# Kernel optimization log

Hardware: AMD Instinct MI355X
Metric: run time of the kernel (lower is better)

Reference implementation:

```python
import jax, jax.numpy as jnp
import numpy as np

B, N, D, H, EF = 8, 1024, 768, 8, 4
S = D * EF          # sparse_dim = 3072
HD = S // H         # head_dim = 384
HUB_POW = 1.5
PERSIST = 0.95
EPS = 1e-6
LN_EPS = 1e-5


def setup_inputs() -> dict:
    key = jax.random.key(0)
    ks = jax.random.split(key, 8)
    s = 0.02  # weight init scale
    return {
        "x": jax.random.normal(ks[0], (B, N, D), jnp.float32),
        "memory": jax.random.normal(ks[1], (H, HD, HD), jnp.float32) * 0.01,
        "ln_g": jnp.ones((D,), jnp.float32),
        "ln_b": jnp.zeros((D,), jnp.float32),
        "w_in": jax.random.normal(ks[2], (D, 3 * S), jnp.float32) * s,
        "b_in": jnp.zeros((3 * S,), jnp.float32),
        "w_out": jax.random.normal(ks[3], (S, D), jnp.float32) * s,
        "b_out": jnp.zeros((D,), jnp.float32),
        "w_rg": jax.random.normal(ks[4], (D, H), jnp.float32) * s,
        "b_rg": jnp.zeros((H,), jnp.float32),
        "w_wg": jax.random.normal(ks[5], (D, H), jnp.float32) * s,
        "b_wg": jnp.zeros((H,), jnp.float32),
        "w_res": jax.random.normal(ks[6], (D, 1), jnp.float32) * s,
        "b_res": jnp.zeros((1,), jnp.float32),
    }


def reference(x, memory, ln_g, ln_b, w_in, b_in, w_out, b_out,
              w_rg, b_rg, w_wg, b_wg, w_res, b_res):
    residual = x
    # LayerNorm (biased variance, matching torch)
    mu = x.mean(axis=-1, keepdims=True)
    var = x.var(axis=-1, keepdims=True)
    xn = (x - mu) / jnp.sqrt(var + LN_EPS) * ln_g + ln_b

    qkv = xn @ w_in + b_in                      # [B,N,3S]
    q, k, v = jnp.split(qkv, 3, axis=-1)

    def to_heads(t):                            # [B,N,S] -> [B,H,N,hd]
        return t.reshape(B, N, H, HD).transpose(0, 2, 1, 3)

    # power-law hub feature map
    q = jnp.power(jax.nn.relu(to_heads(q)) + EPS, HUB_POW)
    k = jnp.power(jax.nn.relu(to_heads(k)) + EPS, HUB_POW)
    v = to_heads(v)
    # normalize k over the token axis
    k = k / (k.sum(axis=2, keepdims=True) + EPS)

    # per-head linear-attention state: k^T @ v -> [B,H,hd,hd]
    batch_state = jnp.einsum('bhnd,bhne->bhde', k, v)

    x_mean = xn.mean(axis=1)                    # [B,D]
    read = jax.nn.sigmoid(x_mean @ w_rg + b_rg)[:, :, None, None]   # [B,H,1,1]
    write = jax.nn.sigmoid(x_mean @ w_wg + b_wg)[:, :, None, None]  # [B,H,1,1]
    residue = jax.nn.sigmoid(xn @ w_res + b_res)                    # [B,N,1]

    # gated EMA memory update (update happens BEFORE read, as in source)
    state_mean = batch_state.mean(axis=0)       # [H,hd,hd]
    mem_new = PERSIST * memory + (1.0 - PERSIST) * write.mean(axis=0) * state_mean

    # read from updated persistent memory
    y = jnp.einsum('bhnd,bhde->bhne', q, mem_new[None] * read)
    y = y.transpose(0, 2, 1, 3).reshape(B, N, S)

    out = residue * (y @ w_out + b_out) + (1.0 - residue) * residual
    return out
```

## Files before the change

### kernel.cpp

```cpp
#include <hip/hip_runtime.h>
#include <hip/hip_bf16.h>
#include <cstdint>
#include <cstddef>


typedef __bf16 bf16_t;
typedef bf16_t bf16x4 __attribute__((ext_vector_type(4)));
typedef bf16_t bf16x8 __attribute__((ext_vector_type(8)));
typedef float f32x4 __attribute__((ext_vector_type(4)));

__device__ __forceinline__ void gemm128_bt(
    const bf16_t* __restrict__ A, int lda,
    const bf16_t* __restrict__ BT, int ldb,
    int K, int row0, int col0,
    bf16_t* As, bf16_t* Bs, f32x4 acc[4][4])
{
    const int t    = threadIdx.x;
    const int lane = t & 63;
    const int wid  = t >> 6;
    const int wr   = wid >> 1, wc = wid & 1;
    const int fr   = lane & 15;
    const int fk   = (lane >> 4) * 8;

#pragma unroll
    for (int m = 0; m < 4; ++m)
#pragma unroll
        for (int n = 0; n < 4; ++n)
            acc[m][n] = (f32x4){0.f, 0.f, 0.f, 0.f};

    const int rr = lane >> 2;
    const int rc = (lane & 3) * 8;

    for (int k0 = 0; k0 < K; k0 += 32) {
#pragma unroll
        for (int c = 0; c < 2; ++c) {
            const int q = wid * 2 + c;
            __builtin_amdgcn_global_load_lds(
                (const __attribute__((address_space(1))) void*)(A + (size_t)(row0 + q * 16 + rr) * lda + (k0 + rc)),
                (__attribute__((address_space(3))) void*)(As + q * 512), 16, 0, 0);
            __builtin_amdgcn_global_load_lds(
                (const __attribute__((address_space(1))) void*)(BT + (size_t)(col0 + q * 16 + rr) * ldb + (k0 + rc)),
                (__attribute__((address_space(3))) void*)(Bs + q * 512), 16, 0, 0);
        }
        __syncthreads();

        bf16x8 av[4], bv[4];
#pragma unroll
        for (int m = 0; m < 4; ++m)
            av[m] = *(const bf16x8*)&As[(wr * 64 + m * 16 + fr) * 32 + fk];
#pragma unroll
        for (int n = 0; n < 4; ++n)
            bv[n] = *(const bf16x8*)&Bs[(wc * 64 + n * 16 + fr) * 32 + fk];
#pragma unroll
        for (int m = 0; m < 4; ++m)
#pragma unroll
            for (int n = 0; n < 4; ++n)
                acc[m][n] = __builtin_amdgcn_mfma_f32_16x16x32_bf16(av[m], bv[n], acc[m][n], 0, 0, 0);
        __syncthreads();
    }
}

__device__ __forceinline__ void band_map(int flat, int nby, int& bx, int& by)
{
    const int xcd = flat & 7;
    const int seq = flat >> 3;
    const int bandsz = nby >> 3;
    by = xcd * bandsz + (seq % bandsz);
    bx = seq / bandsz;
}


__global__ void ktrans_w(const float* __restrict__ in, bf16_t* __restrict__ out, int R, int C)
{
    __shared__ float tl[32][33];
    const int c0 = blockIdx.x * 32, r0 = blockIdx.y * 32;
    const int tx = threadIdx.x, ty = threadIdx.y;
#pragma unroll
    for (int i = ty; i < 32; i += 8) tl[i][tx] = in[(size_t)(r0 + i) * C + c0 + tx];
    __syncthreads();
#pragma unroll
    for (int i = ty; i < 32; i += 8) out[(size_t)(c0 + i) * R + r0 + tx] = (bf16_t)tl[tx][i];
}

__device__ __forceinline__ float block_sum256(float v, float* s4)
{
#pragma unroll
    for (int off = 32; off > 0; off >>= 1) v += __shfl_down(v, off);
    const int lane = threadIdx.x & 63, w = threadIdx.x >> 6;
    if (lane == 0) s4[w] = v;
    __syncthreads();
    return s4[0] + s4[1] + s4[2] + s4[3];
}

__global__ void __launch_bounds__(256) kln(
    const float* __restrict__ x, const float* __restrict__ g, const float* __restrict__ bt,
    const float* __restrict__ w_res, const float* __restrict__ b_res,
    bf16_t* __restrict__ xn, float* __restrict__ residue)
{
    __shared__ float red[12];
    const int row = blockIdx.x;
    const float* xr = x + (size_t)row * 768;
    const int t = threadIdx.x;
    const float v0 = xr[t], v1 = xr[t + 256], v2 = xr[t + 512];
    const float ts  = block_sum256(v0 + v1 + v2, red);
    const float ts2 = block_sum256(v0 * v0 + v1 * v1 + v2 * v2, red + 4);
    const float mu  = ts * (1.f / 768.f);
    const float var = ts2 * (1.f / 768.f) - mu * mu;
    const float rs  = rsqrtf(var + 1e-5f);
    float dot = 0.f;
    {
        float xv;
        xv = (v0 - mu) * rs * g[t]       + bt[t];       xn[(size_t)row * 768 + t]       = (bf16_t)xv; dot += xv * w_res[t];
        xv = (v1 - mu) * rs * g[t + 256] + bt[t + 256]; xn[(size_t)row * 768 + t + 256] = (bf16_t)xv; dot += xv * w_res[t + 256];
        xv = (v2 - mu) * rs * g[t + 512] + bt[t + 512]; xn[(size_t)row * 768 + t + 512] = (bf16_t)xv; dot += xv * w_res[t + 512];
    }
    const float td = block_sum256(dot, red + 8);
    if (t == 0) residue[row] = 1.f / (1.f + expf(-(td + b_res[0])));
}

__global__ void kcolmean(const bf16_t* __restrict__ xn, float* __restrict__ xmean)
{
    const int b = blockIdx.x, dc = blockIdx.y, nc = blockIdx.z;
    const int d = dc * 256 + threadIdx.x;
    const bf16_t* p = xn + (size_t)(b * 1024 + nc * 128) * 768 + d;
    float s = 0.f;
#pragma unroll 4
    for (int n = 0; n < 128; ++n) s += (float)p[(size_t)n * 768];
    atomicAdd(&xmean[b * 768 + d], s);
}

__global__ void __launch_bounds__(256) kgates(
    const float* __restrict__ xmean,
    const float* __restrict__ w_rg, const float* __restrict__ b_rg,
    const float* __restrict__ w_wg, const float* __restrict__ b_wg,
    float* __restrict__ read_g, float* __restrict__ wmean)
{
    __shared__ float pr[64][4], pw[64][4], wg[64];
    const int t = threadIdx.x, grp = t >> 2, qtr = t & 3;
    const int b = grp >> 3, h = grp & 7;
    float dr = 0.f, dw = 0.f;
    for (int d = qtr * 192; d < qtr * 192 + 192; ++d) {
        const float xm = xmean[b * 768 + d] * (1.f / 1024.f);
        dr += xm * w_rg[d * 8 + h];
        dw += xm * w_wg[d * 8 + h];
    }
    pr[grp][qtr] = dr; pw[grp][qtr] = dw;
    __syncthreads();
    if (qtr == 0) {
        const float sr = pr[grp][0] + pr[grp][1] + pr[grp][2] + pr[grp][3];
        const float sw = pw[grp][0] + pw[grp][1] + pw[grp][2] + pw[grp][3];
        read_g[grp] = 1.f / (1.f + expf(-(sr + b_rg[h])));
        wg[grp]     = 1.f / (1.f + expf(-(sw + b_wg[h])));
    }
    __syncthreads();
    if (t < 8) {
        float s = 0.f;
#pragma unroll
        for (int b2 = 0; b2 < 8; ++b2) s += wg[b2 * 8 + t];
        wmean[t] = s * 0.125f;
    }
}

__global__ void __launch_bounds__(512, 2) kgemm_qkv256(
    const bf16_t* __restrict__ xnc, const bf16_t* __restrict__ w_inT,
    const float* __restrict__ b_in,
    bf16_t* __restrict__ qfc, bf16_t* __restrict__ kTc, bf16_t* __restrict__ vTc,
    float* __restrict__ ksum_c, int nrt )
{
    __shared__ __align__(16) bf16_t L[65536];
    const int t = threadIdx.x, lane = t & 63, wid = t >> 6;
    const int wr = wid >> 2, wc = wid & 3;
    int bx, by;
    band_map(blockIdx.y * 36 + blockIdx.x, nrt, bx, by);
    const int row0 = by * 256, col0 = bx * 256;

    f32x4 acc[8][4];
#pragma unroll
    for (int m = 0; m < 8; ++m)
#pragma unroll
        for (int n = 0; n < 4; ++n)
            acc[m][n] = (f32x4){0.f, 0.f, 0.f, 0.f};

    const int grow = 16 * wid + (lane >> 2);
    const int gcol = (lane & 3) * 8;
    const int ldst = 512 * wid + 8 * lane;

    auto stage = [&](int buf, int k0) {
        bf16_t* base = &L[buf * 32768];
#pragma unroll
        for (int op = 0; op < 2; ++op) {
            const bf16_t* src = op ? w_inT : xnc;
            const int r0 = op ? col0 : row0;
#pragma unroll
            for (int s = 0; s < 2; ++s)
#pragma unroll
                for (int j = 0; j < 2; ++j)
                    __builtin_amdgcn_global_load_lds(
                        (const __attribute__((address_space(1))) void*)(src + (size_t)(r0 + 128 * j + grow) * 768 + (k0 + 32 * s + gcol)),
                        (__attribute__((address_space(3))) void*)(base + op * 16384 + s * 8192 + j * 4096 + ldst),
                        16, 0, 0);
        }
    };

    const int fr = lane & 15, fo = (lane >> 4) * 8;

    stage(0, 0);
    __syncthreads();
    int cur = 0;
    for (int k0 = 0; k0 < 768; k0 += 64) {
        if (k0 + 64 < 768) stage(cur ^ 1, k0 + 64);
        const bf16_t* base = &L[cur * 32768];
#pragma unroll
        for (int s = 0; s < 2; ++s) {
            bf16x8 bv[4];
#pragma unroll
            for (int n = 0; n < 4; ++n)
                bv[n] = *(const bf16x8*)&base[16384 + s * 8192 + (wc * 64 + n * 16 + fr) * 32 + fo];
#pragma unroll
            for (int m = 0; m < 8; ++m) {
                const bf16x8 av = *(const bf16x8*)&base[s * 8192 + (wr * 128 + m * 16 + fr) * 32 + fo];
#pragma unroll
                for (int n = 0; n < 4; ++n)
                    acc[m][n] = __builtin_amdgcn_mfma_f32_16x16x32_bf16(av, bv[n], acc[m][n], 0, 0, 0);
            }
        }
        __syncthreads();
        cur ^= 1;
    }

    const int third = col0 / 3072;
    if (third == 0) {
#pragma unroll
        for (int m = 0; m < 8; ++m) {
#pragma unroll
            for (int n2 = 0; n2 < 4; ++n2) {
                const int col  = col0 + wc * 64 + n2 * 16 + fr;
                const float bias = b_in[col];
#pragma unroll
                for (int r = 0; r < 4; ++r) {
                    const int row = row0 + wr * 128 + m * 16 + (lane >> 4) * 4 + r;
                    const float v = acc[m][n2][r] + bias;
                    const float u = fmaxf(v, 0.f) + 1e-6f;
                    qfc[(size_t)row * 3072 + col] = (bf16_t)(u * sqrtf(u));
                }
            }
        }
    } else {
        const int lb  = row0 >> 10;
        const int nbb = (row0 & 1023) + wr * 128 + (lane >> 4) * 4;
#pragma unroll
        for (int n2 = 0; n2 < 4; ++n2) {
            const int colg = col0 + wc * 64 + n2 * 16 + fr;
            const int coll = colg - third * 3072;
            const int h = coll / 384, d = coll % 384;
            bf16_t* dstT = ((third == 1) ? kTc : vTc) + (size_t)(lb * 8 + h) * 393216;
            const float bias = b_in[colg];
            float ksp = 0.f;
#pragma unroll
            for (int m = 0; m < 8; ++m) {
                bf16x4 pk;
#pragma unroll
                for (int r = 0; r < 4; ++r) {
                    float v = acc[m][n2][r] + bias;
                    if (third == 1) { const float u = fmaxf(v, 0.f) + 1e-6f; v = u * sqrtf(u); ksp += v; }
                    pk[r] = (bf16_t)v;
                }
                *(bf16x4*)&dstT[(size_t)d * 1024 + nbb + m * 16] = pk;
            }
            if (third == 1) atomicAdd(&ksum_c[(size_t)(lb * 8 + h) * 384 + d], ksp);
        }
    }
}

__global__ void __launch_bounds__(256) kgemm_state(
    const bf16_t* __restrict__ kTc, const bf16_t* __restrict__ vTc,
    const float* __restrict__ ksum_c, float* __restrict__ ssum)
{
    __shared__ __align__(16) bf16_t As[4096], Bs[4096];
    const int lbh = blockIdx.z, h = lbh & 7;
    const int row0 = blockIdx.y * 128, col0 = blockIdx.x * 128;
    const bf16_t* A  = kTc + (size_t)lbh * 393216;
    const bf16_t* BT = vTc + (size_t)lbh * 393216;
    f32x4 acc[4][4];
    gemm128_bt(A, 1024, BT, 1024, 1024, row0, col0, As, Bs, acc);

    const int lane = threadIdx.x & 63, wid = threadIdx.x >> 6;
    const int wr = wid >> 1, wc = wid & 1;
    float* ss = ssum + (size_t)h * 147456;
#pragma unroll
    for (int m = 0; m < 4; ++m) {
#pragma unroll
        for (int r = 0; r < 4; ++r) {
            const int d = row0 + wr * 64 + m * 16 + (lane >> 4) * 4 + r;
            const float sc = 1.f / (ksum_c[(size_t)lbh * 384 + d] + 1e-6f);
#pragma unroll
            for (int n = 0; n < 4; ++n) {
                const int e = col0 + wc * 64 + n * 16 + (lane & 15);
                atomicAdd(&ss[(size_t)d * 384 + e], acc[m][n][r] * sc);
            }
        }
    }
}

__global__ void kmemupd(const float* __restrict__ mem, const float* __restrict__ ssum,
                        const float* __restrict__ wmean, bf16_t* __restrict__ memT)
{
    __shared__ float tl[32][33];
    const int h = blockIdx.z;
    const int e0 = blockIdx.x * 32, d0 = blockIdx.y * 32;
    const int tx = threadIdx.x, ty = threadIdx.y;
    const size_t base = (size_t)h * 147456;
    const float wm = wmean[h] * (0.05f / 8.f);
#pragma unroll
    for (int i = ty; i < 32; i += 8) {
        const size_t idx = base + (size_t)(d0 + i) * 384 + e0 + tx;
        tl[i][tx] = 0.95f * mem[idx] + wm * ssum[idx];
    }
    __syncthreads();
#pragma unroll
    for (int i = ty; i < 32; i += 8)
        memT[base + (size_t)(e0 + i) * 384 + d0 + tx] = (bf16_t)tl[tx][i];
}

__global__ void __launch_bounds__(256) kgemm_y(
    const bf16_t* __restrict__ qf, const bf16_t* __restrict__ memT,
    const float* __restrict__ read_g, bf16_t* __restrict__ yf)
{
    __shared__ __align__(16) bf16_t As[4096], Bs[4096];
    const int bh = blockIdx.z, b = bh >> 3, h = bh & 7;
    const int row0 = blockIdx.y * 128, col0 = blockIdx.x * 128;
    const bf16_t* A  = qf + (size_t)b * 1024 * 3072 + (size_t)h * 384;
    const bf16_t* BT = memT + (size_t)h * 147456;
    f32x4 acc[4][4];
    gemm128_bt(A, 3072, BT, 384, 384, row0, col0, As, Bs, acc);

    const float rg = read_g[bh];
    const int lane = threadIdx.x & 63, wid = threadIdx.x >> 6;
    const int wr = wid >> 1, wc = wid & 1;
#pragma unroll
    for (int m = 0; m < 4; ++m) {
#pragma unroll
        for (int n = 0; n < 4; ++n) {
            const int col = col0 + wc * 64 + n * 16 + (lane & 15);
#pragma unroll
            for (int r = 0; r < 4; ++r) {
                const int row = row0 + wr * 64 + m * 16 + (lane >> 4) * 4 + r;
                yf[(size_t)(b * 1024 + row) * 3072 + h * 384 + col] = (bf16_t)(acc[m][n][r] * rg);
            }
        }
    }
}

__global__ void __launch_bounds__(256) kgemm_out(
    const bf16_t* __restrict__ yf, const bf16_t* __restrict__ w_outT,
    const float* __restrict__ b_out, const float* __restrict__ residue,
    const float* __restrict__ x, float* __restrict__ out)
{
    __shared__ __align__(16) bf16_t As[4096], Bs[4096];
    int bx, by;
    band_map(blockIdx.y * 6 + blockIdx.x, 64, bx, by);
    const int row0 = by * 128, col0 = bx * 128;
    f32x4 acc[4][4];
    gemm128_bt(yf, 3072, w_outT, 3072, 3072, row0, col0, As, Bs, acc);

    const int lane = threadIdx.x & 63, wid = threadIdx.x >> 6;
    const int wr = wid >> 1, wc = wid & 1;
#pragma unroll
    for (int m = 0; m < 4; ++m) {
#pragma unroll
        for (int n = 0; n < 4; ++n) {
            const int col = col0 + wc * 64 + n * 16 + (lane & 15);
            const float bias = b_out[col];
#pragma unroll
            for (int r = 0; r < 4; ++r) {
                const int row = row0 + wr * 64 + m * 16 + (lane >> 4) * 4 + r;
                const float v = acc[m][n][r] + bias;
                const float rr = residue[row];
                out[(size_t)row * 768 + col] = rr * v + (1.f - rr) * x[(size_t)row * 768 + col];
            }
        }
    }
}

extern "C" void kernel_launch(void* const* d_in, const int* in_sizes, int n_in,
                              void* d_out, int out_size, void* d_ws, size_t ws_size,
                              hipStream_t stream)
{
    (void)in_sizes; (void)n_in; (void)out_size;
    const float* x     = (const float*)d_in[0];
    const float* mem   = (const float*)d_in[1];
    const float* ln_g  = (const float*)d_in[2];
    const float* ln_b  = (const float*)d_in[3];
    const float* w_in  = (const float*)d_in[4];
    const float* b_in  = (const float*)d_in[5];
    const float* w_out = (const float*)d_in[6];
    const float* b_out = (const float*)d_in[7];
    const float* w_rg  = (const float*)d_in[8];
    const float* b_rg  = (const float*)d_in[9];
    const float* w_wg  = (const float*)d_in[10];
    const float* b_wg  = (const float*)d_in[11];
    const float* w_res = (const float*)d_in[12];
    const float* b_res = (const float*)d_in[13];
    float* out = (float*)d_out;

    auto total_for = [&](int c) -> size_t {
        size_t o = 0;
        auto a = [&](size_t b) { o += (b + 255) & ~(size_t)255; };
        a(50331648);
        a(14155776); a(12582912);
        a((size_t)c * 6291456);
        a((size_t)c * 6291456);
        a(4718592); a(4718592); a(2359296);
        a(32768); a(24576); a(98304); a(256); a(256);
        return o;
    };
    int CHUNK = 0;
    for (int c = 8; c >= 2; c >>= 1) if (total_for(c) <= ws_size) { CHUNK = c; break; }
    if (CHUNK == 0) return;

    char* ws = (char*)d_ws;
    size_t off = 0;
    auto alloc = [&](size_t bytes) -> char* {
        char* p = ws + off; off += (bytes + 255) & ~(size_t)255; return p;
    };
    bf16_t* qf     = (bf16_t*)alloc(50331648);
    bf16_t* yf     = (bf16_t*)(ws + off);
    bf16_t* w_inT  = (bf16_t*)alloc(14155776);
    bf16_t* xn     = (bf16_t*)alloc(12582912);
    bf16_t* kTc    = (bf16_t*)alloc((size_t)CHUNK * 6291456);
    bf16_t* vTc    = (bf16_t*)alloc((size_t)CHUNK * 6291456);
    bf16_t* w_outT = (bf16_t*)alloc(4718592);
    float*  ssum   = (float*) alloc(4718592);
    bf16_t* memT   = (bf16_t*)alloc(2359296);
    float*  residue= (float*) alloc(32768);
    float*  xmean  = (float*) alloc(24576);
    float*  ksum   = (float*) alloc(98304);
    float*  read_g = (float*) alloc(256);
    float*  wmean  = (float*) alloc(256);

    hipMemsetAsync(xmean, 0, 24576, stream);
    hipMemsetAsync(ksum,  0, 98304, stream);
    hipMemsetAsync(ssum,  0, 4718592, stream);

    ktrans_w<<<dim3(288, 24), dim3(32, 8), 0, stream>>>(w_in, w_inT, 768, 9216);
    ktrans_w<<<dim3(24, 96), dim3(32, 8), 0, stream>>>(w_out, w_outT, 3072, 768);
    kln<<<8192, 256, 0, stream>>>(x, ln_g, ln_b, w_res, b_res, xn, residue);
    kcolmean<<<dim3(8, 3, 8), 256, 0, stream>>>(xn, xmean);
    kgates<<<1, 256, 0, stream>>>(xmean, w_rg, b_rg, w_wg, b_wg, read_g, wmean);

    const int NC = 8 / CHUNK;
    for (int c = 0; c < NC; ++c) {
        const int b0 = c * CHUNK;
        kgemm_qkv256<<<dim3(36, CHUNK * 4), 512, 0, stream>>>(
            xn + (size_t)b0 * 1024 * 768, w_inT, b_in,
            qf + (size_t)b0 * 1024 * 3072, kTc, vTc,
            ksum + (size_t)b0 * 8 * 384, CHUNK * 4);
        kgemm_state<<<dim3(3, 3, CHUNK * 8), 256, 0, stream>>>(
            kTc, vTc, ksum + (size_t)b0 * 8 * 384, ssum);
    }

    kmemupd<<<dim3(12, 12, 8), dim3(32, 8), 0, stream>>>(mem, ssum, wmean, memT);
    kgemm_y<<<dim3(3, 8, 64), 256, 0, stream>>>(qf, memT, read_g, yf);
    kgemm_out<<<dim3(6, 64), 256, 0, stream>>>(yf, w_outT, b_out, residue, x, out);
}
```

Measured before the change: 405.0 us.

## Reassociate memory read with output projection to drop per-batch y GEMM

Instead of computing y = q·(mem_new·read) per batch and head and then projecting with w_out, the code first forms G = mem_new·w_out per head (a small GEMM over 768 output columns) and then runs the output GEMM directly on q. The read gate is folded into q in the QKV epilogue, and the memory update becomes a plain elementwise kernel with no transpose. This removes the large 64-block y GEMM and the yf round trip through memory. In exchange it adds one small GEMM and stores q scaled by the gate in bf16, which slightly changes rounding.

```diff
diff --git a/kernel.cpp b/kernel.cpp
--- a/kernel.cpp
+++ b/kernel.cpp
@@ -8,6 +8,9 @@
 typedef bf16_t bf16x4 __attribute__((ext_vector_type(4)));
 typedef bf16_t bf16x8 __attribute__((ext_vector_type(8)));
 typedef float f32x4 __attribute__((ext_vector_type(4)));
+
+#define AS1 __attribute__((address_space(1)))
+#define AS3 __attribute__((address_space(3)))
 
 __device__ __forceinline__ void gemm128_bt(
     const bf16_t* __restrict__ A, int lda,
@@ -36,11 +39,11 @@
         for (int c = 0; c < 2; ++c) {
             const int q = wid * 2 + c;
             __builtin_amdgcn_global_load_lds(
-                (const __attribute__((address_space(1))) void*)(A + (size_t)(row0 + q * 16 + rr) * lda + (k0 + rc)),
-                (__attribute__((address_space(3))) void*)(As + q * 512), 16, 0, 0);
+                (const AS1 void*)(A + (size_t)(row0 + q * 16 + rr) * lda + (k0 + rc)),
+                (AS3 void*)(As + q * 512), 16, 0, 0);
             __builtin_amdgcn_global_load_lds(
-                (const __attribute__((address_space(1))) void*)(BT + (size_t)(col0 + q * 16 + rr) * ldb + (k0 + rc)),
-                (__attribute__((address_space(3))) void*)(Bs + q * 512), 16, 0, 0);
+                (const AS1 void*)(BT + (size_t)(col0 + q * 16 + rr) * ldb + (k0 + rc)),
+                (AS3 void*)(Bs + q * 512), 16, 0, 0);
         }
         __syncthreads();
 
@@ -163,7 +166,7 @@
 
 __global__ void __launch_bounds__(512, 2) kgemm_qkv256(
     const bf16_t* __restrict__ xnc, const bf16_t* __restrict__ w_inT,
-    const float* __restrict__ b_in,
+    const float* __restrict__ b_in, const float* __restrict__ rg_c,
     bf16_t* __restrict__ qfc, bf16_t* __restrict__ kTc, bf16_t* __restrict__ vTc,
     float* __restrict__ ksum_c, int nrt )
 {
@@ -196,8 +199,8 @@
 #pragma unroll
                 for (int j = 0; j < 2; ++j)
                     __builtin_amdgcn_global_load_lds(
-                        (const __attribute__((address_space(1))) void*)(src + (size_t)(r0 + 128 * j + grow) * 768 + (k0 + 32 * s + gcol)),
-                        (__attribute__((address_space(3))) void*)(base + op * 16384 + s * 8192 + j * 4096 + ldst),
+                        (const AS1 void*)(src + (size_t)(r0 + 128 * j + grow) * 768 + (k0 + 32 * s + gcol)),
+                        (AS3 void*)(base + op * 16384 + s * 8192 + j * 4096 + ldst),
                         16, 0, 0);
         }
     };
@@ -229,24 +232,26 @@
     }
 
     const int third = col0 / 3072;
+    const int lb = row0 >> 10;
     if (third == 0) {
 #pragma unroll
-        for (int m = 0; m < 8; ++m) {
-#pragma unroll
-            for (int n2 = 0; n2 < 4; ++n2) {
-                const int col  = col0 + wc * 64 + n2 * 16 + fr;
-                const float bias = b_in[col];
+        for (int n2 = 0; n2 < 4; ++n2) {
+            const int col  = col0 + wc * 64 + n2 * 16 + fr;
+            const int h    = col / 384;
+            const float rg = rg_c[lb * 8 + h];
+            const float bias = b_in[col];
+#pragma unroll
+            for (int m = 0; m < 8; ++m) {
 #pragma unroll
                 for (int r = 0; r < 4; ++r) {
                     const int row = row0 + wr * 128 + m * 16 + (lane >> 4) * 4 + r;
                     const float v = acc[m][n2][r] + bias;
                     const float u = fmaxf(v, 0.f) + 1e-6f;
-                    qfc[(size_t)row * 3072 + col] = (bf16_t)(u * sqrtf(u));
+                    qfc[(size_t)row * 3072 + col] = (bf16_t)(rg * u * sqrtf(u));
                 }
             }
         }
     } else {
-        const int lb  = row0 >> 10;
         const int nbb = (row0 & 1023) + wr * 128 + (lane >> 4) * 4;
 #pragma unroll
         for (int n2 = 0; n2 < 4; ++n2) {
@@ -302,57 +307,44 @@
     }
 }
 
-__global__ void kmemupd(const float* __restrict__ mem, const float* __restrict__ ssum,
-                        const float* __restrict__ wmean, bf16_t* __restrict__ memT)
-{
-    __shared__ float tl[32][33];
+__global__ void kmemupd_ew(const float* __restrict__ mem, const float* __restrict__ ssum,
+                           const float* __restrict__ wmean, bf16_t* __restrict__ mem_new)
+{
+    const int idx = blockIdx.x * 256 + threadIdx.x;
+    const int h = idx / 147456;
+    const float wm = wmean[h] * (0.05f / 8.f);
+    mem_new[idx] = (bf16_t)(0.95f * mem[idx] + wm * ssum[idx]);
+}
+
+__global__ void __launch_bounds__(256) kgemm_G(
+    const bf16_t* __restrict__ w_outT, const bf16_t* __restrict__ mem_new,
+    bf16_t* __restrict__ GT)
+{
+    __shared__ __align__(16) bf16_t As[4096], Bs[4096];
     const int h = blockIdx.z;
-    const int e0 = blockIdx.x * 32, d0 = blockIdx.y * 32;
-    const int tx = threadIdx.x, ty = threadIdx.y;
-    const size_t base = (size_t)h * 147456;
-    const float wm = wmean[h] * (0.05f / 8.f);
-#pragma unroll
-    for (int i = ty; i < 32; i += 8) {
-        const size_t idx = base + (size_t)(d0 + i) * 384 + e0 + tx;
-        tl[i][tx] = 0.95f * mem[idx] + wm * ssum[idx];
-    }
-    __syncthreads();
-#pragma unroll
-    for (int i = ty; i < 32; i += 8)
-        memT[base + (size_t)(e0 + i) * 384 + d0 + tx] = (bf16_t)tl[tx][i];
-}
-
-__global__ void __launch_bounds__(256) kgemm_y(
-    const bf16_t* __restrict__ qf, const bf16_t* __restrict__ memT,
-    const float* __restrict__ read_g, bf16_t* __restrict__ yf)
-{
-    __shared__ __align__(16) bf16_t As[4096], Bs[4096];
-    const int bh = blockIdx.z, b = bh >> 3, h = bh & 7;
     const int row0 = blockIdx.y * 128, col0 = blockIdx.x * 128;
-    const bf16_t* A  = qf + (size_t)b * 1024 * 3072 + (size_t)h * 384;
-    const bf16_t* BT = memT + (size_t)h * 147456;
     f32x4 acc[4][4];
-    gemm128_bt(A, 3072, BT, 384, 384, row0, col0, As, Bs, acc);
-
-    const float rg = read_g[bh];
+    gemm128_bt(w_outT + h * 384, 3072, mem_new + (size_t)h * 147456, 384,
+               384, row0, col0, As, Bs, acc);
+
     const int lane = threadIdx.x & 63, wid = threadIdx.x >> 6;
     const int wr = wid >> 1, wc = wid & 1;
 #pragma unroll
     for (int m = 0; m < 4; ++m) {
 #pragma unroll
         for (int n = 0; n < 4; ++n) {
-            const int col = col0 + wc * 64 + n * 16 + (lane & 15);
+            const int d = col0 + wc * 64 + n * 16 + (lane & 15);
 #pragma unroll
             for (int r = 0; r < 4; ++r) {
-                const int row = row0 + wr * 64 + m * 16 + (lane >> 4) * 4 + r;
-                yf[(size_t)(b * 1024 + row) * 3072 + h * 384 + col] = (bf16_t)(acc[m][n][r] * rg);
+                const int c = row0 + wr * 64 + m * 16 + (lane >> 4) * 4 + r;
+                GT[(size_t)c * 3072 + h * 384 + d] = (bf16_t)acc[m][n][r];
             }
         }
     }
 }
 
 __global__ void __launch_bounds__(256) kgemm_out(
-    const bf16_t* __restrict__ yf, const bf16_t* __restrict__ w_outT,
+    const bf16_t* __restrict__ qf, const bf16_t* __restrict__ GT,
     const float* __restrict__ b_out, const float* __restrict__ residue,
     const float* __restrict__ x, float* __restrict__ out)
 {
@@ -361,7 +353,7 @@
     band_map(blockIdx.y * 6 + blockIdx.x, 64, bx, by);
     const int row0 = by * 128, col0 = bx * 128;
     f32x4 acc[4][4];
-    gemm128_bt(yf, 3072, w_outT, 3072, 3072, row0, col0, As, Bs, acc);
+    gemm128_bt(qf, 3072, GT, 3072, 3072, row0, col0, As, Bs, acc);
 
     const int lane = threadIdx.x & 63, wid = threadIdx.x >> 6;
     const int wr = wid >> 1, wc = wid & 1;
@@ -423,20 +415,20 @@
     auto alloc = [&](size_t bytes) -> char* {
         char* p = ws + off; off += (bytes + 255) & ~(size_t)255; return p;
     };
-    bf16_t* qf     = (bf16_t*)alloc(50331648);
-    bf16_t* yf     = (bf16_t*)(ws + off);
-    bf16_t* w_inT  = (bf16_t*)alloc(14155776);
-    bf16_t* xn     = (bf16_t*)alloc(12582912);
-    bf16_t* kTc    = (bf16_t*)alloc((size_t)CHUNK * 6291456);
-    bf16_t* vTc    = (bf16_t*)alloc((size_t)CHUNK * 6291456);
-    bf16_t* w_outT = (bf16_t*)alloc(4718592);
-    float*  ssum   = (float*) alloc(4718592);
-    bf16_t* memT   = (bf16_t*)alloc(2359296);
-    float*  residue= (float*) alloc(32768);
-    float*  xmean  = (float*) alloc(24576);
-    float*  ksum   = (float*) alloc(98304);
-    float*  read_g = (float*) alloc(256);
-    float*  wmean  = (float*) alloc(256);
+    bf16_t* qf      = (bf16_t*)alloc(50331648);
+    bf16_t* w_inT   = (bf16_t*)alloc(14155776);
+    bf16_t* GT      = w_inT;
+    bf16_t* xn      = (bf16_t*)alloc(12582912);
+    bf16_t* kTc     = (bf16_t*)alloc((size_t)CHUNK * 6291456);
+    bf16_t* vTc     = (bf16_t*)alloc((size_t)CHUNK * 6291456);
+    bf16_t* w_outT  = (bf16_t*)alloc(4718592);
+    float*  ssum    = (float*) alloc(4718592);
+    bf16_t* mem_new = (bf16_t*)alloc(2359296);
+    float*  residue = (float*) alloc(32768);
+    float*  xmean   = (float*) alloc(24576);
+    float*  ksum    = (float*) alloc(98304);
+    float*  read_g  = (float*) alloc(256);
+    float*  wmean   = (float*) alloc(256);
 
     hipMemsetAsync(xmean, 0, 24576, stream);
     hipMemsetAsync(ksum,  0, 98304, stream);
@@ -452,14 +444,14 @@
     for (int c = 0; c < NC; ++c) {
         const int b0 = c * CHUNK;
         kgemm_qkv256<<<dim3(36, CHUNK * 4), 512, 0, stream>>>(
-            xn + (size_t)b0 * 1024 * 768, w_inT, b_in,
+            xn + (size_t)b0 * 1024 * 768, w_inT, b_in, read_g + b0 * 8,
             qf + (size_t)b0 * 1024 * 3072, kTc, vTc,
             ksum + (size_t)b0 * 8 * 384, CHUNK * 4);
         kgemm_state<<<dim3(3, 3, CHUNK * 8), 256, 0, stream>>>(
             kTc, vTc, ksum + (size_t)b0 * 8 * 384, ssum);
     }
 
-    kmemupd<<<dim3(12, 12, 8), dim3(32, 8), 0, stream>>>(mem, ssum, wmean, memT);
-    kgemm_y<<<dim3(3, 8, 64), 256, 0, stream>>>(qf, memT, read_g, yf);
-    kgemm_out<<<dim3(6, 64), 256, 0, stream>>>(yf, w_outT, b_out, residue, x, out);
-}
+    kmemupd_ew<<<4608, 256, 0, stream>>>(mem, ssum, wmean, mem_new);
+    kgemm_G<<<dim3(3, 6, 8), 256, 0, stream>>>(w_outT, mem_new, GT);
+    kgemm_out<<<dim3(6, 64), 256, 0, stream>>>(qf, GT, b_out, residue, x, out);
+}
```

Measured after the change: 375.6 us. 7.3% less time.
